# Optimization experiments

Measured on AMD Instinct MI355X. Metric: run time of the kernel, lower is better.

Reference implementation:

```python
import jax, jax.numpy as jnp
import numpy as np

N, F_IN, F_OUT, N_HEAD = 4096, 256, 64, 4
EDGE_P = 0.01  # sparsity of the random adjacency


def setup_inputs() -> dict:
    key = jax.random.key(0)
    k_h, k_adj, k_w, k_as, k_ad = jax.random.split(key, 5)
    h = jax.random.normal(k_h, (N, F_IN), dtype=jnp.float32)
    # random boolean adjacency with self-loops so every softmax row is valid
    adj = jax.random.uniform(k_adj, (N, N)) < EDGE_P
    adj = adj | jnp.eye(N, dtype=bool)
    # xavier_uniform-style params
    lim_w = float(np.sqrt(6.0 / (F_IN + F_OUT)))
    lim_a = float(np.sqrt(6.0 / (F_OUT + 1)))
    w = jax.random.uniform(k_w, (N_HEAD, F_IN, F_OUT), minval=-lim_w, maxval=lim_w, dtype=jnp.float32)
    a_src = jax.random.uniform(k_as, (N_HEAD, F_OUT, 1), minval=-lim_a, maxval=lim_a, dtype=jnp.float32)
    a_dst = jax.random.uniform(k_ad, (N_HEAD, F_OUT, 1), minval=-lim_a, maxval=lim_a, dtype=jnp.float32)
    bias = jnp.zeros((F_OUT,), dtype=jnp.float32)
    return {"h": h, "adj": adj, "w": w, "a_src": a_src, "a_dst": a_dst, "bias": bias}


def reference(h, adj, w, a_src, a_dst, bias):
    # h_prime[k] = h @ w[k]  -> [H, n, f_out]
    h_prime = jnp.einsum('nf,hfo->hno', h, w)
    # attention logits: attn[k,i,j] = src[k,i] + dst[k,j]
    src = jnp.einsum('hno,ho->hn', h_prime, a_src[..., 0])  # [H, n]
    dst = jnp.einsum('hno,ho->hn', h_prime, a_dst[..., 0])  # [H, n]
    scores = src[:, :, None] + dst[:, None, :]              # [H, n, n]
    scores = jnp.where(scores >= 0, scores, 0.2 * scores)   # leaky_relu(0.2)
    neg = jnp.asarray(jnp.finfo(scores.dtype).min, scores.dtype)
    scores = jnp.where(adj[None, :, :], scores, neg)
    attn = jax.nn.softmax(scores, axis=-1)                  # [H, n, n]
    out = jnp.einsum('hij,hjo->iho', attn, h_prime)         # [n, H, f_out]
    return out + bias
```

## Files before the change

### kernel.cpp

```cpp
#include <hip/hip_runtime.h>

#define NN 4096
#define FIN 256
#define FOUT 64
#define NH 4
#define CAP 128
#define WROW 258

typedef __attribute__((ext_vector_type(8))) short bf16x8;
typedef __attribute__((ext_vector_type(4))) float f32x4;

__device__ __forceinline__ unsigned short f2bf(float f) {
    unsigned u = __float_as_uint(f);
    u = (u + 0x7fff + ((u >> 16) & 1)) >> 16;
    return (unsigned short)u;
}
__device__ __forceinline__ float bf2f(unsigned short s) {
    return __uint_as_float((unsigned)s << 16);
}
__device__ __forceinline__ int mbcnt64(unsigned long long m) {
    return __builtin_amdgcn_mbcnt_hi((unsigned)(m >> 32),
           __builtin_amdgcn_mbcnt_lo((unsigned)m, 0));
}

__global__ __launch_bounds__(256) void gat_hprime(
    const float* __restrict__ h, const float* __restrict__ w,
    const float* __restrict__ a_src, const float* __restrict__ a_dst,
    unsigned short* __restrict__ hb, float* __restrict__ sd)
{
    const int b = blockIdx.x, t = threadIdx.x;
    const int head = b & 3, n0 = (b >> 2) * 32;
    const int wv = t >> 6, lane = t & 63;
    const int lrow = lane & 15, lk8 = lane >> 4;

    __shared__ __align__(16) unsigned short ws[64 * WROW];
    __shared__ float sdbuf[2][2][16][2];

#pragma unroll
    for (int i = 0; i < 16; ++i) {
        const int k  = (t >> 4) + i * 16;
        const int o4 = (t & 15) * 4;
        const float4 v = *(const float4*)(w + ((size_t)head * FIN + k) * FOUT + o4);
        ws[(o4 + 0) * WROW + k] = f2bf(v.x);
        ws[(o4 + 1) * WROW + k] = f2bf(v.y);
        ws[(o4 + 2) * WROW + k] = f2bf(v.z);
        ws[(o4 + 3) * WROW + k] = f2bf(v.w);
    }

    const float* hrow = h + (size_t)(n0 + (wv >> 1) * 16 + lrow) * FIN + lk8 * 8;
    bf16x8 a[8];
#pragma unroll
    for (int ks = 0; ks < 8; ++ks) {
        const float4 v0 = *(const float4*)(hrow + ks * 32);
        const float4 v1 = *(const float4*)(hrow + ks * 32 + 4);
        union { bf16x8 v; unsigned short s[8]; } u;
        u.s[0] = f2bf(v0.x); u.s[1] = f2bf(v0.y);
        u.s[2] = f2bf(v0.z); u.s[3] = f2bf(v0.w);
        u.s[4] = f2bf(v1.x); u.s[5] = f2bf(v1.y);
        u.s[6] = f2bf(v1.z); u.s[7] = f2bf(v1.w);
        a[ks] = u.v;
    }
    __syncthreads();

    const int obase = (wv & 1) * 32;
    f32x4 acc[2] = {{0.f,0.f,0.f,0.f},{0.f,0.f,0.f,0.f}};
#pragma unroll
    for (int ks = 0; ks < 8; ++ks) {
#pragma unroll
        for (int nt = 0; nt < 2; ++nt) {
            const bf16x8 bf = *(const bf16x8*)
                &ws[(obase + nt * 16 + lrow) * WROW + ks * 32 + lk8 * 8];
            acc[nt] = __builtin_amdgcn_mfma_f32_16x16x32_bf16(a[ks], bf, acc[nt], 0, 0, 0);
        }
    }

    const int mbase = n0 + (wv >> 1) * 16 + lk8 * 4;
#pragma unroll
    for (int nt = 0; nt < 2; ++nt)
#pragma unroll
        for (int r = 0; r < 4; ++r)
            hb[((size_t)head * NN + mbase + r) * FOUT + obase + nt * 16 + lrow] =
                f2bf(acc[nt][r]);

    float as_nt[2], ad_nt[2];
#pragma unroll
    for (int nt = 0; nt < 2; ++nt) {
        as_nt[nt] = a_src[head * FOUT + obase + nt * 16 + lrow];
        ad_nt[nt] = a_dst[head * FOUT + obase + nt * 16 + lrow];
    }
    float psr[4] = {0.f,0.f,0.f,0.f}, pdr[4] = {0.f,0.f,0.f,0.f};
#pragma unroll
    for (int nt = 0; nt < 2; ++nt)
#pragma unroll
        for (int r = 0; r < 4; ++r) {
            psr[r] = fmaf(acc[nt][r], as_nt[nt], psr[r]);
            pdr[r] = fmaf(acc[nt][r], ad_nt[nt], pdr[r]);
        }
#pragma unroll
    for (int r = 0; r < 4; ++r)
#pragma unroll
        for (int off = 1; off <= 8; off <<= 1) {
            psr[r] += __shfl_xor(psr[r], off, 64);
            pdr[r] += __shfl_xor(pdr[r], off, 64);
        }
    if (lrow == 0)
#pragma unroll
        for (int r = 0; r < 4; ++r) {
            sdbuf[wv >> 1][wv & 1][lk8 * 4 + r][0] = psr[r];
            sdbuf[wv >> 1][wv & 1][lk8 * 4 + r][1] = pdr[r];
        }
    __syncthreads();
    if ((wv & 1) == 0 && lrow == 0) {
        const int p = wv >> 1;
#pragma unroll
        for (int r = 0; r < 4; ++r) {
            const int n = lk8 * 4 + r;
            const int node = n0 + p * 16 + n;
            sd[(size_t)node * 8 + head]     = sdbuf[p][0][n][0] + sdbuf[p][1][n][0];
            sd[(size_t)node * 8 + 4 + head] = sdbuf[p][0][n][1] + sdbuf[p][1][n][1];
        }
    }
}

__global__ __launch_bounds__(256) void gat_attn(
    const int* __restrict__ adj, const unsigned short* __restrict__ hb,
    const float* __restrict__ sd, const float* __restrict__ bias,
    float* __restrict__ out)
{
    const int i = blockIdx.x, t = threadIdx.x, wv = t >> 6, lane = t & 63;

    __shared__ int   idx_l[CAP];
    __shared__ float sc[NH][CAP];
    __shared__ int   ccnt[16];
    __shared__ float inv_sum[NH];
    __shared__ float accbuf[4][64][4];

    const int4* arow = (const int4*)(adj + (size_t)i * NN);
    int4 a[4];
#pragma unroll
    for (int it = 0; it < 4; ++it) a[it] = arow[wv * 256 + it * 64 + lane];

    int myoff[4];
#pragma unroll
    for (int it = 0; it < 4; ++it) {
        const unsigned long long b0 = __ballot(a[it].x != 0);
        const unsigned long long b1 = __ballot(a[it].y != 0);
        const unsigned long long b2 = __ballot(a[it].z != 0);
        const unsigned long long b3 = __ballot(a[it].w != 0);
        myoff[it] = mbcnt64(b0) + mbcnt64(b1) + mbcnt64(b2) + mbcnt64(b3);
        if (lane == 0)
            ccnt[wv * 4 + it] = __popcll(b0) + __popcll(b1) +
                                __popcll(b2) + __popcll(b3);
    }
    __syncthreads();

    int cb[4];
    int s = 0;
#pragma unroll
    for (int k = 0; k < 16; ++k) {
        if ((k >> 2) == wv) cb[k & 3] = s;
        s += ccnt[k];
    }
    const int count = min(s, CAP);

#pragma unroll
    for (int it = 0; it < 4; ++it) {
        int p = cb[it] + myoff[it];
        const int col0 = (wv * 256 + it * 64 + lane) * 4;
        if (a[it].x) { if (p < CAP) idx_l[p] = col0;     ++p; }
        if (a[it].y) { if (p < CAP) idx_l[p] = col0 + 1; ++p; }
        if (a[it].z) { if (p < CAP) idx_l[p] = col0 + 2; ++p; }
        if (a[it].w) { if (p < CAP) idx_l[p] = col0 + 3; ++p; }
    }
    __syncthreads();

    if (t < count) {
        const int j = idx_l[t];
        const float4 sv = *(const float4*)(sd + (size_t)i * 8);
        const float4 dv = *(const float4*)(sd + (size_t)j * 8 + 4);
        const float s0 = sv.x + dv.x, s1 = sv.y + dv.y;
        const float s2 = sv.z + dv.z, s3 = sv.w + dv.w;
        sc[0][t] = (s0 >= 0.f) ? s0 : 0.2f * s0;
        sc[1][t] = (s1 >= 0.f) ? s1 : 0.2f * s1;
        sc[2][t] = (s2 >= 0.f) ? s2 : 0.2f * s2;
        sc[3][t] = (s3 >= 0.f) ? s3 : 0.2f * s3;
    }
    __syncthreads();

    {
        float m = -3.4e38f;
        for (int p = lane; p < count; p += 64) m = fmaxf(m, sc[wv][p]);
#pragma unroll
        for (int off = 32; off >= 1; off >>= 1) m = fmaxf(m, __shfl_xor(m, off, 64));
        float e = 0.f;
        for (int p = lane; p < count; p += 64) {
            const float v = __expf(sc[wv][p] - m);
            sc[wv][p] = v;
            e += v;
        }
#pragma unroll
        for (int off = 32; off >= 1; off >>= 1) e += __shfl_xor(e, off, 64);
        if (lane == 0) inv_sum[wv] = 1.f / e;
    }
    __syncthreads();

    const int hh = lane >> 4, og = lane & 15;
    const unsigned short* hpb = hb + (size_t)hh * NN * FOUT + og * 4;
    float4 accv = make_float4(0.f, 0.f, 0.f, 0.f);
    for (int p0 = wv; p0 < count; p0 += 16) {
        int jj[4]; float ee[4]; ushort4 hv[4];
#pragma unroll
        for (int k = 0; k < 4; ++k) {
            const int pp = p0 + k * 4;
            const bool act = pp < count;
            jj[k] = act ? idx_l[pp] : 0;
            ee[k] = act ? sc[hh][pp] : 0.f;
        }
#pragma unroll
        for (int k = 0; k < 4; ++k)
            hv[k] = *(const ushort4*)(hpb + (size_t)jj[k] * FOUT);
#pragma unroll
        for (int k = 0; k < 4; ++k) {
            accv.x = fmaf(ee[k], bf2f(hv[k].x), accv.x);
            accv.y = fmaf(ee[k], bf2f(hv[k].y), accv.y);
            accv.z = fmaf(ee[k], bf2f(hv[k].z), accv.z);
            accv.w = fmaf(ee[k], bf2f(hv[k].w), accv.w);
        }
    }
    *(float4*)&accbuf[wv][lane][0] = accv;
    __syncthreads();

    if (wv == 0) {
        float4 r0 = *(const float4*)&accbuf[0][lane][0];
        const float4 r1 = *(const float4*)&accbuf[1][lane][0];
        const float4 r2 = *(const float4*)&accbuf[2][lane][0];
        const float4 r3 = *(const float4*)&accbuf[3][lane][0];
        r0.x += r1.x + r2.x + r3.x;
        r0.y += r1.y + r2.y + r3.y;
        r0.z += r1.z + r2.z + r3.z;
        r0.w += r1.w + r2.w + r3.w;
        const float is = inv_sum[hh];
        const float4 bv = *(const float4*)(bias + og * 4);
        float4 o;
        o.x = r0.x * is + bv.x;
        o.y = r0.y * is + bv.y;
        o.z = r0.z * is + bv.z;
        o.w = r0.w * is + bv.w;
        *(float4*)(out + (size_t)i * (NH * FOUT) + hh * FOUT + og * 4) = o;
    }
}

extern "C" void kernel_launch(void* const* d_in, const int* in_sizes, int n_in,
                              void* d_out, int out_size, void* d_ws, size_t ws_size,
                              hipStream_t stream) {
    const float* h     = (const float*)d_in[0];
    const int*   adj   = (const int*)d_in[1];
    const float* w     = (const float*)d_in[2];
    const float* a_src = (const float*)d_in[3];
    const float* a_dst = (const float*)d_in[4];
    const float* bias  = (const float*)d_in[5];
    float* out = (float*)d_out;

    unsigned short* hb = (unsigned short*)d_ws;
    float* sd          = (float*)(hb + (size_t)NH * NN * FOUT);

    gat_hprime<<<512, 256, 0, stream>>>(h, w, a_src, a_dst, hb, sd);
    gat_attn<<<NN, 256, 0, stream>>>(adj, hb, sd, bias, out);
}
```

Measured before the change: 34.65 us.

## Split each attention row across two blocks with flash-style partial softmax merge

The attention kernel now launches two blocks per row, each scanning half of the adjacency row, computing a local max, sum and unnormalized weighted accumulation. A new merge kernel combines the two halves with rescaled exponentials, normalizes, and adds the bias. This doubles parallelism and halves the per-block adjacency scan latency. In exchange it adds a third launch and writes and rereads partial results through global memory. Per-half capacity also drops to 96 neighbours, with padding of the index and score buffers.

```diff
diff --git a/kernel.cpp b/kernel.cpp
--- a/kernel.cpp
+++ b/kernel.cpp
@@ -4,7 +4,7 @@
 #define FIN 256
 #define FOUT 64
 #define NH 4
-#define CAP 128
+#define CAP2 96
 #define WROW 258
 
 typedef __attribute__((ext_vector_type(8))) short bf16x8;
@@ -122,61 +122,63 @@
     }
 }
 
-__global__ __launch_bounds__(256) void gat_attn(
+__global__ __launch_bounds__(256) void gat_part(
     const int* __restrict__ adj, const unsigned short* __restrict__ hb,
-    const float* __restrict__ sd, const float* __restrict__ bias,
-    float* __restrict__ out)
+    const float* __restrict__ sd,
+    float* __restrict__ pacc, float* __restrict__ ms)
 {
-    const int i = blockIdx.x, t = threadIdx.x, wv = t >> 6, lane = t & 63;
-
-    __shared__ int   idx_l[CAP];
-    __shared__ float sc[NH][CAP];
-    __shared__ int   ccnt[16];
-    __shared__ float inv_sum[NH];
+    const int b = blockIdx.x, t = threadIdx.x, wv = t >> 6, lane = t & 63;
+    const int r = b >> 1, half = b & 1;
+
+    __shared__ int   idx_l[CAP2 + 16];
+    __shared__ float sc[NH][CAP2 + 16];
+    __shared__ int   ccnt[8];
+    __shared__ float mloc[NH], sloc[NH];
     __shared__ float accbuf[4][64][4];
 
-    const int4* arow = (const int4*)(adj + (size_t)i * NN);
-    int4 a[4];
-#pragma unroll
-    for (int it = 0; it < 4; ++it) a[it] = arow[wv * 256 + it * 64 + lane];
-
-    int myoff[4];
-#pragma unroll
-    for (int it = 0; it < 4; ++it) {
+    const int4* arow = (const int4*)(adj + (size_t)r * NN + half * 2048);
+    int4 a[2];
+#pragma unroll
+    for (int it = 0; it < 2; ++it) a[it] = arow[wv * 128 + it * 64 + lane];
+
+    int myoff[2];
+#pragma unroll
+    for (int it = 0; it < 2; ++it) {
         const unsigned long long b0 = __ballot(a[it].x != 0);
         const unsigned long long b1 = __ballot(a[it].y != 0);
         const unsigned long long b2 = __ballot(a[it].z != 0);
         const unsigned long long b3 = __ballot(a[it].w != 0);
         myoff[it] = mbcnt64(b0) + mbcnt64(b1) + mbcnt64(b2) + mbcnt64(b3);
         if (lane == 0)
-            ccnt[wv * 4 + it] = __popcll(b0) + __popcll(b1) +
+            ccnt[wv * 2 + it] = __popcll(b0) + __popcll(b1) +
                                 __popcll(b2) + __popcll(b3);
     }
     __syncthreads();
 
-    int cb[4];
+    int cb[2];
     int s = 0;
 #pragma unroll
-    for (int k = 0; k < 16; ++k) {
-        if ((k >> 2) == wv) cb[k & 3] = s;
+    for (int k = 0; k < 8; ++k) {
+        if ((k >> 1) == wv) cb[k & 1] = s;
         s += ccnt[k];
     }
-    const int count = min(s, CAP);
-
-#pragma unroll
-    for (int it = 0; it < 4; ++it) {
+    const int count = min(s, CAP2);
+    const int cpad  = (count + 7) & ~7;
+
+#pragma unroll
+    for (int it = 0; it < 2; ++it) {
         int p = cb[it] + myoff[it];
-        const int col0 = (wv * 256 + it * 64 + lane) * 4;
-        if (a[it].x) { if (p < CAP) idx_l[p] = col0;     ++p; }
-        if (a[it].y) { if (p < CAP) idx_l[p] = col0 + 1; ++p; }
-        if (a[it].z) { if (p < CAP) idx_l[p] = col0 + 2; ++p; }
-        if (a[it].w) { if (p < CAP) idx_l[p] = col0 + 3; ++p; }
+        const int col0 = half * 2048 + (wv * 128 + it * 64 + lane) * 4;
+        if (a[it].x) { if (p < CAP2) idx_l[p] = col0;     ++p; }
+        if (a[it].y) { if (p < CAP2) idx_l[p] = col0 + 1; ++p; }
+        if (a[it].z) { if (p < CAP2) idx_l[p] = col0 + 2; ++p; }
+        if (a[it].w) { if (p < CAP2) idx_l[p] = col0 + 3; ++p; }
     }
     __syncthreads();
 
     if (t < count) {
         const int j = idx_l[t];
-        const float4 sv = *(const float4*)(sd + (size_t)i * 8);
+        const float4 sv = *(const float4*)(sd + (size_t)r * 8);
         const float4 dv = *(const float4*)(sd + (size_t)j * 8 + 4);
         const float s0 = sv.x + dv.x, s1 = sv.y + dv.y;
         const float s2 = sv.z + dv.z, s3 = sv.w + dv.w;
@@ -184,6 +186,10 @@
         sc[1][t] = (s1 >= 0.f) ? s1 : 0.2f * s1;
         sc[2][t] = (s2 >= 0.f) ? s2 : 0.2f * s2;
         sc[3][t] = (s3 >= 0.f) ? s3 : 0.2f * s3;
+    } else if (t < cpad + 12 && t < CAP2 + 16) {
+        idx_l[t] = 0;
+#pragma unroll
+        for (int hh = 0; hh < NH; ++hh) sc[hh][t] = 0.f;
     }
     __syncthreads();
 
@@ -200,7 +206,7 @@
         }
 #pragma unroll
         for (int off = 32; off >= 1; off >>= 1) e += __shfl_xor(e, off, 64);
-        if (lane == 0) inv_sum[wv] = 1.f / e;
+        if (lane == 0) { mloc[wv] = m; sloc[wv] = e; }
     }
     __syncthreads();
 
@@ -239,15 +245,30 @@
         r0.y += r1.y + r2.y + r3.y;
         r0.z += r1.z + r2.z + r3.z;
         r0.w += r1.w + r2.w + r3.w;
-        const float is = inv_sum[hh];
-        const float4 bv = *(const float4*)(bias + og * 4);
-        float4 o;
-        o.x = r0.x * is + bv.x;
-        o.y = r0.y * is + bv.y;
-        o.z = r0.z * is + bv.z;
-        o.w = r0.w * is + bv.w;
-        *(float4*)(out + (size_t)i * (NH * FOUT) + hh * FOUT + og * 4) = o;
-    }
+        *(float4*)(pacc + (size_t)b * 256 + hh * 64 + og * 4) = r0;
+        if (lane < 4)      ms[(size_t)b * 8 + lane]     = mloc[lane];
+        else if (lane < 8) ms[(size_t)b * 8 + lane]     = sloc[lane - 4];
+    }
+}
+
+__global__ __launch_bounds__(256) void gat_merge(
+    const float* __restrict__ pacc, const float* __restrict__ ms,
+    const float* __restrict__ bias, float* __restrict__ out)
+{
+    const int r = blockIdx.x, t = threadIdx.x;
+    const int hh = t >> 6, o = t & 63;
+
+    const float m0 = ms[(size_t)(r * 2 + 0) * 8 + hh];
+    const float s0 = ms[(size_t)(r * 2 + 0) * 8 + 4 + hh];
+    const float m1 = ms[(size_t)(r * 2 + 1) * 8 + hh];
+    const float s1 = ms[(size_t)(r * 2 + 1) * 8 + 4 + hh];
+    const float m  = fmaxf(m0, m1);
+    const float w0 = __expf(m0 - m), w1 = __expf(m1 - m);
+    const float inv = 1.f / (w0 * s0 + w1 * s1);
+
+    const float p0 = pacc[(size_t)(r * 2 + 0) * 256 + t];
+    const float p1 = pacc[(size_t)(r * 2 + 1) * 256 + t];
+    out[(size_t)r * 256 + t] = (w0 * p0 + w1 * p1) * inv + bias[o];
 }
 
 extern "C" void kernel_launch(void* const* d_in, const int* in_sizes, int n_in,
@@ -262,8 +283,11 @@
     float* out = (float*)d_out;
 
     unsigned short* hb = (unsigned short*)d_ws;
-    float* sd          = (float*)(hb + (size_t)NH * NN * FOUT);
+    float* sd   = (float*)(hb + (size_t)NH * NN * FOUT);
+    float* pacc = sd + (size_t)NN * 8;
+    float* ms   = pacc + (size_t)NN * 2 * 256;
 
     gat_hprime<<<512, 256, 0, stream>>>(h, w, a_src, a_dst, hb, sd);
-    gat_attn<<<NN, 256, 0, stream>>>(adj, hb, sd, bias, out);
-}
+    gat_part<<<NN * 2, 256, 0, stream>>>(adj, hb, sd, pacc, ms);
+    gat_merge<<<NN, 256, 0, stream>>>(pacc, ms, bias, out);
+}
```

After: 39.08 us. +12.8%, slower.

## Compress adjacency to bitmasks in prep kernel alongside h_prime blocks

Applied to the files above, without the earlier changes.

Extra blocks are added to the first kernel that stream the 64MB int adjacency matrix and pack it into per-row 64-bit ballot masks, so this scan runs concurrently with the h_prime GEMM blocks. The attention kernel then reads only 512 bytes of bits per row and builds the neighbour index list with a single-wave prefix scan and ffs loop. The full adjacency read still happens, but it now overlaps the GEMM and is done in a grid-stride streaming pattern. The cost is an extra bitmask write/read and a serial per-lane bit loop.

```diff
diff --git a/kernel.cpp b/kernel.cpp
--- a/kernel.cpp
+++ b/kernel.cpp
@@ -6,6 +6,8 @@
 #define NH 4
 #define CAP 128
 #define WROW 258
+#define HPB 512
+#define SCB 2048
 
 typedef __attribute__((ext_vector_type(8))) short bf16x8;
 typedef __attribute__((ext_vector_type(4))) float f32x4;
@@ -18,23 +20,42 @@
 __device__ __forceinline__ float bf2f(unsigned short s) {
     return __uint_as_float((unsigned)s << 16);
 }
-__device__ __forceinline__ int mbcnt64(unsigned long long m) {
-    return __builtin_amdgcn_mbcnt_hi((unsigned)(m >> 32),
-           __builtin_amdgcn_mbcnt_lo((unsigned)m, 0));
-}
-
-__global__ __launch_bounds__(256) void gat_hprime(
-    const float* __restrict__ h, const float* __restrict__ w,
-    const float* __restrict__ a_src, const float* __restrict__ a_dst,
-    unsigned short* __restrict__ hb, float* __restrict__ sd)
+
+__global__ __launch_bounds__(256) void gat_prep(
+    const float* __restrict__ h, const int* __restrict__ adj,
+    const float* __restrict__ w, const float* __restrict__ a_src,
+    const float* __restrict__ a_dst,
+    unsigned short* __restrict__ hb, float* __restrict__ sd,
+    unsigned long long* __restrict__ bits)
 {
     const int b = blockIdx.x, t = threadIdx.x;
-    const int head = b & 3, n0 = (b >> 2) * 32;
     const int wv = t >> 6, lane = t & 63;
-    const int lrow = lane & 15, lk8 = lane >> 4;
 
     __shared__ __align__(16) unsigned short ws[64 * WROW];
     __shared__ float sdbuf[2][2][16][2];
+
+    if (b >= HPB) {
+        const int nvec = NN * NN / 4;
+        const int step = SCB * 256;
+        for (int g = (b - HPB) * 256 + t; g < nvec; g += step) {
+            const int4 a = ((const int4*)adj)[g];
+            const unsigned long long b0 = __ballot(a.x != 0);
+            const unsigned long long b1 = __ballot(a.y != 0);
+            const unsigned long long b2 = __ballot(a.z != 0);
+            const unsigned long long b3 = __ballot(a.w != 0);
+            const int row = g >> 10;
+            const int it  = (g >> 6) & 15;
+            unsigned long long mk = b0;
+            mk = ((lane & 3) == 1) ? b1 : mk;
+            mk = ((lane & 3) == 2) ? b2 : mk;
+            mk = ((lane & 3) == 3) ? b3 : mk;
+            if (lane < 4) bits[(size_t)row * 64 + it * 4 + lane] = mk;
+        }
+        return;
+    }
+
+    const int head = b & 3, n0 = (b >> 2) * 32;
+    const int lrow = lane & 15, lk8 = lane >> 4;
 
 #pragma unroll
     for (int i = 0; i < 16; ++i) {
@@ -123,56 +144,40 @@
 }
 
 __global__ __launch_bounds__(256) void gat_attn(
-    const int* __restrict__ adj, const unsigned short* __restrict__ hb,
-    const float* __restrict__ sd, const float* __restrict__ bias,
-    float* __restrict__ out)
+    const unsigned long long* __restrict__ bits,
+    const unsigned short* __restrict__ hb, const float* __restrict__ sd,
+    const float* __restrict__ bias, float* __restrict__ out)
 {
     const int i = blockIdx.x, t = threadIdx.x, wv = t >> 6, lane = t & 63;
 
     __shared__ int   idx_l[CAP];
     __shared__ float sc[NH][CAP];
-    __shared__ int   ccnt[16];
+    __shared__ int   cnt;
     __shared__ float inv_sum[NH];
     __shared__ float accbuf[4][64][4];
 
-    const int4* arow = (const int4*)(adj + (size_t)i * NN);
-    int4 a[4];
-#pragma unroll
-    for (int it = 0; it < 4; ++it) a[it] = arow[wv * 256 + it * 64 + lane];
-
-    int myoff[4];
-#pragma unroll
-    for (int it = 0; it < 4; ++it) {
-        const unsigned long long b0 = __ballot(a[it].x != 0);
-        const unsigned long long b1 = __ballot(a[it].y != 0);
-        const unsigned long long b2 = __ballot(a[it].z != 0);
-        const unsigned long long b3 = __ballot(a[it].w != 0);
-        myoff[it] = mbcnt64(b0) + mbcnt64(b1) + mbcnt64(b2) + mbcnt64(b3);
-        if (lane == 0)
-            ccnt[wv * 4 + it] = __popcll(b0) + __popcll(b1) +
-                                __popcll(b2) + __popcll(b3);
-    }
-    __syncthreads();
-
-    int cb[4];
-    int s = 0;
-#pragma unroll
-    for (int k = 0; k < 16; ++k) {
-        if ((k >> 2) == wv) cb[k & 3] = s;
-        s += ccnt[k];
-    }
-    const int count = min(s, CAP);
-
-#pragma unroll
-    for (int it = 0; it < 4; ++it) {
-        int p = cb[it] + myoff[it];
-        const int col0 = (wv * 256 + it * 64 + lane) * 4;
-        if (a[it].x) { if (p < CAP) idx_l[p] = col0;     ++p; }
-        if (a[it].y) { if (p < CAP) idx_l[p] = col0 + 1; ++p; }
-        if (a[it].z) { if (p < CAP) idx_l[p] = col0 + 2; ++p; }
-        if (a[it].w) { if (p < CAP) idx_l[p] = col0 + 3; ++p; }
-    }
-    __syncthreads();
+    if (wv == 0) {
+        unsigned long long m = bits[(size_t)i * 64 + lane];
+        const int c = __popcll(m);
+        int pre = c;
+#pragma unroll
+        for (int off = 1; off < 64; off <<= 1) {
+            const int nb = __shfl_up(pre, off, 64);
+            if (lane >= off) pre += nb;
+        }
+        int p = pre - c;
+        const int cb = (lane >> 2) * 256 + (lane & 3);
+        while (m) {
+            const int bpos = __ffsll((unsigned long long)m) - 1;
+            if (p < CAP) idx_l[p] = cb + 4 * bpos;
+            ++p;
+            m &= m - 1;
+        }
+        if (lane == 63) cnt = pre;
+    }
+    __syncthreads();
+
+    const int count = min(cnt, CAP);
 
     if (t < count) {
         const int j = idx_l[t];
@@ -263,7 +268,8 @@
 
     unsigned short* hb = (unsigned short*)d_ws;
     float* sd          = (float*)(hb + (size_t)NH * NN * FOUT);
-
-    gat_hprime<<<512, 256, 0, stream>>>(h, w, a_src, a_dst, hb, sd);
-    gat_attn<<<NN, 256, 0, stream>>>(adj, hb, sd, bias, out);
-}
+    unsigned long long* bits = (unsigned long long*)(sd + (size_t)NN * 8);
+
+    gat_prep<<<HPB + SCB, 256, 0, stream>>>(h, adj, w, a_src, a_dst, hb, sd, bits);
+    gat_attn<<<NN, 256, 0, stream>>>(bits, hb, sd, bias, out);
+}
```

New measurement: 35.28 us. Within noise of the previous version (+1.8%).
